# Performance work log

Measured on AMD Instinct MI355X. Metric: run time of the kernel, lower is better.

## Reference

```python
import jax, jax.numpy as jnp
import numpy as np

MAX_DIST = 5
D_PE = 16
NUM_ENTITIES = 50000
NUM_EDGES = 800000
NUM_ANCHOR_TRIPLES = 32
MAX_SOURCES = 2 * NUM_ANCHOR_TRIPLES  # upper bound on unique anchor entities


def setup_inputs() -> dict:
    key = jax.random.key(0)
    k1, k2, k3, k4 = jax.random.split(key, 4)
    h_ids = jax.random.randint(k1, (NUM_EDGES,), 0, NUM_ENTITIES)
    t_ids = jax.random.randint(k2, (NUM_EDGES,), 0, NUM_ENTITIES)
    anchor_triple_indices = jax.random.randint(k3, (NUM_ANCHOR_TRIPLES,), 0, NUM_EDGES)
    dist_embed = jax.random.normal(k4, (MAX_DIST + 1, D_PE), dtype=jnp.float32)
    return {
        "h_ids": h_ids,
        "t_ids": t_ids,
        "anchor_triple_indices": anchor_triple_indices,
        "num_entities": NUM_ENTITIES,
        "dist_embed": dist_embed,
    }


def _bfs_mean_counts(h_ids, t_ids, anchor_triple_indices, num_entities):
    """Returns [num_entities, MAX_DIST+1] mean one-hot distance counts over anchors."""
    # unique anchor entities, padded with -1 to a static size (torch.unique equivalent)
    anchor_ents = jnp.concatenate([h_ids[anchor_triple_indices], t_ids[anchor_triple_indices]])
    sources = jnp.unique(anchor_ents, size=MAX_SOURCES, fill_value=-1)  # [K], sorted
    valid = sources >= 0                                                # [K]
    src = jnp.where(valid, sources, 0)
    K = src.shape[0]
    col = jnp.arange(K)

    # symmetric adjacency as edge list (duplicates are harmless: only >0 is tested)
    edge_src = jnp.concatenate([h_ids, t_ids])  # [2E]
    edge_dst = jnp.concatenate([t_ids, h_ids])  # [2E]

    frontier = jnp.zeros((num_entities, K), jnp.float32).at[src, col].set(1.0)
    visited = jnp.zeros((num_entities, K), bool).at[src, col].set(True)
    dist = jnp.full((num_entities, K), MAX_DIST, jnp.int32).at[src, col].set(0)

    for depth in range(1, MAX_DIST + 1):  # fixed small hop count
        # sparse adj @ frontier == scatter-add of gathered frontier rows
        new_frontier = jax.ops.segment_sum(frontier[edge_src], edge_dst, num_segments=num_entities)
        newly = (new_frontier > 0) & ~visited
        dist = jnp.where(newly, depth, dist)
        visited = visited | newly
        frontier = newly.astype(jnp.float32)

    # masked mean over valid anchor sources, expressed as distance-count histogram
    w = valid.astype(jnp.float32)
    n_valid = jnp.maximum(w.sum(), 1.0)
    onehot = jax.nn.one_hot(dist, MAX_DIST + 1, dtype=jnp.float32)  # [N, K, D+1]
    counts = jnp.einsum('nkd,k->nd', onehot, w) / n_valid           # [N, D+1]
    return counts


def reference(h_ids, t_ids, anchor_triple_indices, num_entities, dist_embed):
    counts = _bfs_mean_counts(h_ids, t_ids, anchor_triple_indices, num_entities)
    # mean over sources of embed(dist) == counts @ embedding table
    return counts @ dist_embed  # [num_entities, d_pe]
```

## Files before the change

### kernel.cpp

```cpp
#include <hip/hip_runtime.h>
#include <hip/hip_bf16.h>

typedef unsigned long long u64;
typedef unsigned int u32;

#define MAXD 5
#define BSH  6
#define BN   64
#define PAD  16
#define NW   256
#define NTH  256
#define CAPG 2816
#define HEMPTY 0xFFFFFFFFu


__global__ void scatter_setup(const int* __restrict__ h, const int* __restrict__ t,
                              int E, u32* __restrict__ cursorpad,
                              u32* __restrict__ recs, int NB,
                              const int* __restrict__ anchor, int A,
                              u64* __restrict__ NFg, u32* __restrict__ srcPack,
                              int* __restrict__ nvalid) {
    extern __shared__ u32 sh[];
    u32* lh    = sh;
    u32* base  = sh + NB;
    u32* hsKey = sh + 2 * NB;
    u32* hsBit = hsKey + 128;
    int tid = threadIdx.x;

    for (int i = tid; i < NB; i += NTH) lh[i] = 0u;
    if (tid < 128) hsKey[tid] = HEMPTY;
    __syncthreads();

    if (tid < 64) {
        int K = 2 * A;
        int a_ = (tid < K) ? anchor[(tid < A) ? tid : (tid - A)] : 0;
        int my = (tid < K) ? ((tid < A) ? h[a_] : t[a_]) : -1;
        bool uniq = (tid < K);
        for (int j = 0; j < 64; ++j) {
            int o = __shfl(my, j, 64);
            if (j < tid && o == my) uniq = false;
        }
        u64 mask = __ballot(uniq);
        if (blockIdx.x == 0 && tid == 0) *nvalid = (int)__popcll(mask);
        if (uniq) {
            u32 slot = ((u32)my * 2654435761u) >> 25;
            while (atomicCAS(&hsKey[slot], HEMPTY, (u32)my) != HEMPTY)
                slot = (slot + 1) & 127u;
            hsBit[slot] = (u32)tid;
        }
        if (blockIdx.x == 0)
            srcPack[tid] = uniq ? (((u32)my << BSH) | (u32)tid) : HEMPTY;
    }
    __syncthreads();

    auto srcMask = [&](u32 src) -> u64 {
        u32 slot = (src * 2654435761u) >> 25;
        while (true) {
            u32 k = hsKey[slot];
            if (k == src) return 1ull << hsBit[slot];
            if (k == HEMPTY) return 0ull;
            slot = (slot + 1) & 127u;
        }
    };

    int stride = gridDim.x * NTH;
    int t0 = blockIdx.x * NTH + tid;
    for (int e = t0; e < E; e += stride) {
        u32 uu = (u32)h[e], vv = (u32)t[e];
        atomicAdd(&lh[vv >> BSH], 1u);
        atomicAdd(&lh[uu >> BSH], 1u);
    }
    __syncthreads();
    for (int i = tid; i < NB; i += NTH) {
        u32 c = lh[i];
        base[i] = c ? atomicAdd(&cursorpad[i * PAD], c) : 0u;
    }
    __syncthreads();
    for (int i = tid; i < NB; i += NTH) lh[i] = 0u;
    __syncthreads();
    for (int e = t0; e < E; e += stride) {
        u32 uu = (u32)h[e], vv = (u32)t[e];
        u32 b1 = vv >> BSH;
        u32 r1 = base[b1] + atomicAdd(&lh[b1], 1u);
        if (r1 < CAPG) recs[b1 * CAPG + r1] = (uu << BSH) | (vv & (BN - 1));
        u32 b2 = uu >> BSH;
        u32 r2 = base[b2] + atomicAdd(&lh[b2], 1u);
        if (r2 < CAPG) recs[b2 * CAPG + r2] = (vv << BSH) | (uu & (BN - 1));
        if (uu != vv) {
            u64 m1 = srcMask(uu);
            if (m1) atomicOr(&NFg[vv], m1);
            u64 m2 = srcMask(vv);
            if (m2) atomicOr(&NFg[uu], m2);
        }
    }
}

__global__ __launch_bounds__(NTH) void level12(
    const u32* __restrict__ recs, const u32* __restrict__ cursorpad,
    const u32* __restrict__ srcPack, const u64* __restrict__ NFg,
    u64* __restrict__ F2, u64* __restrict__ V, u64* __restrict__ CNT, int N) {
    __shared__ u64 NF[BN];
    __shared__ u32 srcL[64];
    int b = blockIdx.x, tid = threadIdx.x;
    u32 o0 = (u32)b * CAPG;
    u32 cnt = min(cursorpad[b * PAD], (u32)CAPG);
    if (tid < BN) NF[tid] = 0ull;
    if (tid < 64) srcL[tid] = srcPack[tid];
    __syncthreads();
    u32 r = tid;
    for (; r + 3u * NTH < cnt; r += 4u * NTH) {
        u32 c0 = recs[o0 + r],           c1 = recs[o0 + r + NTH];
        u32 c2 = recs[o0 + r + 2 * NTH], c3 = recs[o0 + r + 3 * NTH];
        u64 f0 = NFg[c0 >> BSH], f1 = NFg[c1 >> BSH];
        u64 f2 = NFg[c2 >> BSH], f3 = NFg[c3 >> BSH];
        if (f0) atomicOr(&NF[c0 & (BN - 1)], f0);
        if (f1) atomicOr(&NF[c1 & (BN - 1)], f1);
        if (f2) atomicOr(&NF[c2 & (BN - 1)], f2);
        if (f3) atomicOr(&NF[c3 & (BN - 1)], f3);
    }
    for (; r < cnt; r += NTH) {
        u32 c0 = recs[o0 + r];
        u64 f0 = NFg[c0 >> BSH];
        if (f0) atomicOr(&NF[c0 & (BN - 1)], f0);
    }
    __syncthreads();
    if (tid < BN) {
        int n = b * BN + tid;
        if (n < N) {
            u64 srcbit = 0ull;
            for (int k = 0; k < 64; ++k) {
                u32 p = srcL[k];
                if (p != HEMPTY && (int)(p >> BSH) == n)
                    srcbit |= 1ull << (p & (BN - 1));
            }
            u64 nf1 = NFg[n];
            u64 v1 = srcbit | nf1;
            u64 newly2 = NF[tid] & ~v1;
            V[n] = v1 | newly2;
            F2[n] = newly2;
            CNT[n] = (srcbit ? 1ull : 0ull)
                   | ((u64)__popcll(nf1) << 8)
                   | ((u64)__popcll(newly2) << 16);
        }
    }
}

__global__ __launch_bounds__(NTH) void level3(
    const u32* __restrict__ recs, const u32* __restrict__ cursorpad,
    const u64* __restrict__ Fin, u64* __restrict__ Fout,
    u64* __restrict__ V, u64* __restrict__ CNT, int N) {
    __shared__ u64 NF[BN];
    int b = blockIdx.x, tid = threadIdx.x;
    u32 o0 = (u32)b * CAPG;
    u32 cnt = min(cursorpad[b * PAD], (u32)CAPG);
    if (tid < BN) NF[tid] = 0ull;
    __syncthreads();
    u32 r = tid;
    for (; r + 3u * NTH < cnt; r += 4u * NTH) {
        u32 c0 = recs[o0 + r],           c1 = recs[o0 + r + NTH];
        u32 c2 = recs[o0 + r + 2 * NTH], c3 = recs[o0 + r + 3 * NTH];
        u64 f0 = Fin[c0 >> BSH], f1 = Fin[c1 >> BSH];
        u64 f2 = Fin[c2 >> BSH], f3 = Fin[c3 >> BSH];
        if (f0) atomicOr(&NF[c0 & (BN - 1)], f0);
        if (f1) atomicOr(&NF[c1 & (BN - 1)], f1);
        if (f2) atomicOr(&NF[c2 & (BN - 1)], f2);
        if (f3) atomicOr(&NF[c3 & (BN - 1)], f3);
    }
    for (; r < cnt; r += NTH) {
        u32 c0 = recs[o0 + r];
        u64 f0 = Fin[c0 >> BSH];
        if (f0) atomicOr(&NF[c0 & (BN - 1)], f0);
    }
    __syncthreads();
    if (tid < BN) {
        int n = b * BN + tid;
        if (n < N) {
            u64 vis = V[n];
            u64 newly = NF[tid] & ~vis;
            Fout[n] = newly;
            if (newly) {
                V[n] = vis | newly;
                CNT[n] += (u64)__popcll(newly) << 24;
            }
        }
    }
}

__global__ __launch_bounds__(NTH) void level4_fin(
    const u32* __restrict__ recs, const u32* __restrict__ cursorpad,
    const u64* __restrict__ Fin, const u64* __restrict__ V,
    const u64* __restrict__ CNT, const int* __restrict__ nvalid,
    const float* __restrict__ embed, float* __restrict__ out, int N) {
    __shared__ u64 NF[BN];
    int b = blockIdx.x, tid = threadIdx.x;
    u32 o0 = (u32)b * CAPG;
    u32 cnt = min(cursorpad[b * PAD], (u32)CAPG);
    if (tid < BN) NF[tid] = 0ull;
    __syncthreads();
    u32 r = tid;
    for (; r + 3u * NTH < cnt; r += 4u * NTH) {
        u32 c0 = recs[o0 + r],           c1 = recs[o0 + r + NTH];
        u32 c2 = recs[o0 + r + 2 * NTH], c3 = recs[o0 + r + 3 * NTH];
        u64 f0 = Fin[c0 >> BSH], f1 = Fin[c1 >> BSH];
        u64 f2 = Fin[c2 >> BSH], f3 = Fin[c3 >> BSH];
        if (f0) atomicOr(&NF[c0 & (BN - 1)], f0);
        if (f1) atomicOr(&NF[c1 & (BN - 1)], f1);
        if (f2) atomicOr(&NF[c2 & (BN - 1)], f2);
        if (f3) atomicOr(&NF[c3 & (BN - 1)], f3);
    }
    for (; r < cnt; r += NTH) {
        u32 c0 = recs[o0 + r];
        u64 f0 = Fin[c0 >> BSH];
        if (f0) atomicOr(&NF[c0 & (BN - 1)], f0);
    }
    __syncthreads();
    int nl = tid >> 2, q = tid & 3;
    int n = b * BN + nl;
    if (n >= N) return;
    u64 vis = V[n];
    int c4 = __popcll(NF[nl] & ~vis);
    u64 c = CNT[n];
    int nv = *nvalid;
    float inv = 1.0f / (float)(nv > 0 ? nv : 1);
    float cd[MAXD + 1];
    int total = c4;
#pragma unroll
    for (int d = 0; d < 4; ++d) {
        int x = (int)((c >> (8 * d)) & 0xffull);
        total += x;
        cd[d] = (float)x;
    }
    cd[4] = (float)c4;
    cd[5] = (float)(nv - total);

    const float4* e4 = (const float4*)embed;
    float4 acc = {0.f, 0.f, 0.f, 0.f};
#pragma unroll
    for (int d = 0; d <= MAXD; ++d) {
        float4 e = e4[d * 4 + q];
        acc.x += cd[d] * e.x; acc.y += cd[d] * e.y;
        acc.z += cd[d] * e.z; acc.w += cd[d] * e.w;
    }
    acc.x *= inv; acc.y *= inv; acc.z *= inv; acc.w *= inv;
    ((float4*)(out + (size_t)n * 16))[q] = acc;
}

extern "C" void kernel_launch(void* const* d_in, const int* in_sizes, int n_in,
                              void* d_out, int out_size, void* d_ws, size_t ws_size,
                              hipStream_t stream) {
    const int*   h      = (const int*)d_in[0];
    const int*   t      = (const int*)d_in[1];
    const int*   anchor = (const int*)d_in[2];
    const float* embed  = (const float*)d_in[4];
    float*       out    = (float*)d_out;

    int E = in_sizes[0];
    int A = in_sizes[2];
    int D = in_sizes[4] / (MAXD + 1);
    int N = out_size / D;
    int NB = (N + BN - 1) >> BSH;
    (void)D;

    u32* cursorpad = (u32*)d_ws;
    u64* NFg = (u64*)(cursorpad + (size_t)NB * PAD);
    u64* V   = NFg + N;
    u64* CNT = V + N;
    u64* F2  = CNT + N;
    u64* F3  = F2 + N;
    u32* srcPack = (u32*)(F3 + N);
    int* nvalid  = (int*)(srcPack + 64);
    u32* recs    = (u32*)(nvalid + 1);

    hipMemsetAsync(d_ws, 0, (size_t)NB * PAD * 4 + (size_t)N * 8, stream);

    scatter_setup<<<NW, NTH, (2 * NB + 256) * sizeof(u32), stream>>>(
        h, t, E, cursorpad, recs, NB, anchor, A, NFg, srcPack, nvalid);

    level12<<<NB, NTH, 0, stream>>>(recs, cursorpad, srcPack, NFg, F2, V, CNT, N);
    level3<<<NB, NTH, 0, stream>>>(recs, cursorpad, F2, F3, V, CNT, N);
    level4_fin<<<NB, NTH, 0, stream>>>(recs, cursorpad, F3, V, CNT, nvalid,
                                       embed, out, N);
}
```

Measured before the change: 151.4 us.

## Replace global-atomic bucket scatter with per-chunk shared-memory counting sort

The setup kernel now partitions edges into 512 chunks. Each chunk is counting-sorted by destination bucket in shared memory using a block-wide prefix scan, then written contiguously along with a per-chunk u16 segment offset table. This removes global atomic cursors, the padded cursor array and its memset, and the fixed per-bucket capacity. In exchange, each BFS level kernel must gather its bucket's records from all 512 chunks through short, scattered per-thread segment walks instead of coalesced unrolled streams.

Result: slower. 167.0 us (+10.3%).

```diff
diff --git a/kernel.cpp b/kernel.cpp
--- a/kernel.cpp
+++ b/kernel.cpp
@@ -3,31 +3,33 @@
 
 typedef unsigned long long u64;
 typedef unsigned int u32;
+typedef unsigned short u16;
 
 #define MAXD 5
 #define BSH  6
 #define BN   64
-#define PAD  16
-#define NW   256
+#define NW   512
 #define NTH  256
-#define CAPG 2816
+#define NBMAX 1024
 #define HEMPTY 0xFFFFFFFFu
 
 
-__global__ void scatter_setup(const int* __restrict__ h, const int* __restrict__ t,
-                              int E, u32* __restrict__ cursorpad,
-                              u32* __restrict__ recs, int NB,
-                              const int* __restrict__ anchor, int A,
-                              u64* __restrict__ NFg, u32* __restrict__ srcPack,
-                              int* __restrict__ nvalid) {
+__global__ __launch_bounds__(NTH) void chunk_sort(
+    const int* __restrict__ h, const int* __restrict__ t, int E, int CE, int CAPC,
+    int NB, u32* __restrict__ recs, u16* __restrict__ segtab,
+    const int* __restrict__ anchor, int A,
+    u64* __restrict__ NFg, u32* __restrict__ srcPack, int* __restrict__ nvalid) {
     extern __shared__ u32 sh[];
-    u32* lh    = sh;
-    u32* base  = sh + NB;
-    u32* hsKey = sh + 2 * NB;
+    u32* s     = sh;
+    u32* cur   = sh + NBMAX;
+    u32* hsKey = cur + NB;
     u32* hsBit = hsKey + 128;
-    int tid = threadIdx.x;
-
-    for (int i = tid; i < NB; i += NTH) lh[i] = 0u;
+    u32* buf   = hsBit + 128;
+    int tid = threadIdx.x, c = blockIdx.x;
+    int lo = c * CE, hi = min(E, lo + CE);
+    int nrec = 2 * (hi - lo);
+
+    for (int i = tid; i < NB; i += NTH) cur[i] = 0u;
     if (tid < 128) hsKey[tid] = HEMPTY;
     __syncthreads();
 
@@ -41,16 +43,49 @@
             if (j < tid && o == my) uniq = false;
         }
         u64 mask = __ballot(uniq);
-        if (blockIdx.x == 0 && tid == 0) *nvalid = (int)__popcll(mask);
+        if (c == 0 && tid == 0) *nvalid = (int)__popcll(mask);
         if (uniq) {
             u32 slot = ((u32)my * 2654435761u) >> 25;
             while (atomicCAS(&hsKey[slot], HEMPTY, (u32)my) != HEMPTY)
                 slot = (slot + 1) & 127u;
             hsBit[slot] = (u32)tid;
         }
-        if (blockIdx.x == 0)
+        if (c == 0)
             srcPack[tid] = uniq ? (((u32)my << BSH) | (u32)tid) : HEMPTY;
     }
+    __syncthreads();
+
+    for (int e = lo + tid; e < hi; e += NTH) {
+        u32 uu = (u32)h[e], vv = (u32)t[e];
+        atomicAdd(&cur[vv >> BSH], 1u);
+        atomicAdd(&cur[uu >> BSH], 1u);
+    }
+    __syncthreads();
+
+    for (int k = 0; k < NBMAX / NTH; ++k) {
+        int i = tid + NTH * k;
+        s[i] = (i < NB) ? cur[i] : 0u;
+    }
+    __syncthreads();
+    for (int d = 1; d < NBMAX; d <<= 1) {
+        u32 v0[NBMAX / NTH];
+#pragma unroll
+        for (int k = 0; k < NBMAX / NTH; ++k) {
+            int i = tid + NTH * k;
+            v0[k] = (i >= d) ? s[i - d] : 0u;
+        }
+        __syncthreads();
+#pragma unroll
+        for (int k = 0; k < NBMAX / NTH; ++k) s[tid + NTH * k] += v0[k];
+        __syncthreads();
+    }
+    for (int i = tid; i < NB; i += NTH) {
+        u32 excl = s[i] - cur[i];
+        s[i] = excl;
+        cur[i] = 0u;
+        segtab[c * (NB + 1) + i] = (u16)excl;
+    }
+    if (tid == 0) segtab[c * (NB + 1) + NB] = (u16)nrec;
     __syncthreads();
 
     auto srcMask = [&](u32 src) -> u64 {
@@ -63,29 +98,12 @@
         }
     };
 
-    int stride = gridDim.x * NTH;
-    int t0 = blockIdx.x * NTH + tid;
-    for (int e = t0; e < E; e += stride) {
-        u32 uu = (u32)h[e], vv = (u32)t[e];
-        atomicAdd(&lh[vv >> BSH], 1u);
-        atomicAdd(&lh[uu >> BSH], 1u);
-    }
-    __syncthreads();
-    for (int i = tid; i < NB; i += NTH) {
-        u32 c = lh[i];
-        base[i] = c ? atomicAdd(&cursorpad[i * PAD], c) : 0u;
-    }
-    __syncthreads();
-    for (int i = tid; i < NB; i += NTH) lh[i] = 0u;
-    __syncthreads();
-    for (int e = t0; e < E; e += stride) {
+    for (int e = lo + tid; e < hi; e += NTH) {
         u32 uu = (u32)h[e], vv = (u32)t[e];
         u32 b1 = vv >> BSH;
-        u32 r1 = base[b1] + atomicAdd(&lh[b1], 1u);
-        if (r1 < CAPG) recs[b1 * CAPG + r1] = (uu << BSH) | (vv & (BN - 1));
+        buf[s[b1] + atomicAdd(&cur[b1], 1u)] = (uu << BSH) | (vv & (BN - 1));
         u32 b2 = uu >> BSH;
-        u32 r2 = base[b2] + atomicAdd(&lh[b2], 1u);
-        if (r2 < CAPG) recs[b2 * CAPG + r2] = (vv << BSH) | (uu & (BN - 1));
+        buf[s[b2] + atomicAdd(&cur[b2], 1u)] = (vv << BSH) | (uu & (BN - 1));
         if (uu != vv) {
             u64 m1 = srcMask(uu);
             if (m1) atomicOr(&NFg[vv], m1);
@@ -93,35 +111,31 @@
             if (m2) atomicOr(&NFg[uu], m2);
         }
     }
-}
+    __syncthreads();
+
+    for (int i = tid; i < nrec; i += NTH) recs[c * CAPC + i] = buf[i];
+}
+
 
 __global__ __launch_bounds__(NTH) void level12(
-    const u32* __restrict__ recs, const u32* __restrict__ cursorpad,
+    const u32* __restrict__ recs, const u16* __restrict__ segtab, int CAPC, int NB,
     const u32* __restrict__ srcPack, const u64* __restrict__ NFg,
     u64* __restrict__ F2, u64* __restrict__ V, u64* __restrict__ CNT, int N) {
     __shared__ u64 NF[BN];
     __shared__ u32 srcL[64];
     int b = blockIdx.x, tid = threadIdx.x;
-    u32 o0 = (u32)b * CAPG;
-    u32 cnt = min(cursorpad[b * PAD], (u32)CAPG);
     if (tid < BN) NF[tid] = 0ull;
     if (tid < 64) srcL[tid] = srcPack[tid];
     __syncthreads();
-    u32 r = tid;
-    for (; r + 3u * NTH < cnt; r += 4u * NTH) {
-        u32 c0 = recs[o0 + r],           c1 = recs[o0 + r + NTH];
-        u32 c2 = recs[o0 + r + 2 * NTH], c3 = recs[o0 + r + 3 * NTH];
-        u64 f0 = NFg[c0 >> BSH], f1 = NFg[c1 >> BSH];
-        u64 f2 = NFg[c2 >> BSH], f3 = NFg[c3 >> BSH];
-        if (f0) atomicOr(&NF[c0 & (BN - 1)], f0);
-        if (f1) atomicOr(&NF[c1 & (BN - 1)], f1);
-        if (f2) atomicOr(&NF[c2 & (BN - 1)], f2);
-        if (f3) atomicOr(&NF[c3 & (BN - 1)], f3);
-    }
-    for (; r < cnt; r += NTH) {
-        u32 c0 = recs[o0 + r];
-        u64 f0 = NFg[c0 >> BSH];
-        if (f0) atomicOr(&NF[c0 & (BN - 1)], f0);
+    for (int c = tid; c < NW; c += NTH) {
+        const u16* st = segtab + c * (NB + 1);
+        u32 base = (u32)c * CAPC;
+        u32 k = st[b], k1 = st[b + 1];
+        for (; k < k1; ++k) {
+            u32 rec = recs[base + k];
+            u64 f = NFg[rec >> BSH];
+            if (f) atomicOr(&NF[rec & (BN - 1)], f);
+        }
     }
     __syncthreads();
     if (tid < BN) {
@@ -146,30 +160,22 @@
 }
 
 __global__ __launch_bounds__(NTH) void level3(
-    const u32* __restrict__ recs, const u32* __restrict__ cursorpad,
+    const u32* __restrict__ recs, const u16* __restrict__ segtab, int CAPC, int NB,
     const u64* __restrict__ Fin, u64* __restrict__ Fout,
     u64* __restrict__ V, u64* __restrict__ CNT, int N) {
     __shared__ u64 NF[BN];
     int b = blockIdx.x, tid = threadIdx.x;
-    u32 o0 = (u32)b * CAPG;
-    u32 cnt = min(cursorpad[b * PAD], (u32)CAPG);
     if (tid < BN) NF[tid] = 0ull;
     __syncthreads();
-    u32 r = tid;
-    for (; r + 3u * NTH < cnt; r += 4u * NTH) {
-        u32 c0 = recs[o0 + r],           c1 = recs[o0 + r + NTH];
-        u32 c2 = recs[o0 + r + 2 * NTH], c3 = recs[o0 + r + 3 * NTH];
-        u64 f0 = Fin[c0 >> BSH], f1 = Fin[c1 >> BSH];
-        u64 f2 = Fin[c2 >> BSH], f3 = Fin[c3 >> BSH];
-        if (f0) atomicOr(&NF[c0 & (BN - 1)], f0);
-        if (f1) atomicOr(&NF[c1 & (BN - 1)], f1);
-        if (f2) atomicOr(&NF[c2 & (BN - 1)], f2);
-        if (f3) atomicOr(&NF[c3 & (BN - 1)], f3);
-    }
-    for (; r < cnt; r += NTH) {
-        u32 c0 = recs[o0 + r];
-        u64 f0 = Fin[c0 >> BSH];
-        if (f0) atomicOr(&NF[c0 & (BN - 1)], f0);
+    for (int c = tid; c < NW; c += NTH) {
+        const u16* st = segtab + c * (NB + 1);
+        u32 base = (u32)c * CAPC;
+        u32 k = st[b], k1 = st[b + 1];
+        for (; k < k1; ++k) {
+            u32 rec = recs[base + k];
+            u64 f = Fin[rec >> BSH];
+            if (f) atomicOr(&NF[rec & (BN - 1)], f);
+        }
     }
     __syncthreads();
     if (tid < BN) {
@@ -187,31 +193,23 @@
 }
 
 __global__ __launch_bounds__(NTH) void level4_fin(
-    const u32* __restrict__ recs, const u32* __restrict__ cursorpad,
+    const u32* __restrict__ recs, const u16* __restrict__ segtab, int CAPC, int NB,
     const u64* __restrict__ Fin, const u64* __restrict__ V,
     const u64* __restrict__ CNT, const int* __restrict__ nvalid,
     const float* __restrict__ embed, float* __restrict__ out, int N) {
     __shared__ u64 NF[BN];
     int b = blockIdx.x, tid = threadIdx.x;
-    u32 o0 = (u32)b * CAPG;
-    u32 cnt = min(cursorpad[b * PAD], (u32)CAPG);
     if (tid < BN) NF[tid] = 0ull;
     __syncthreads();
-    u32 r = tid;
-    for (; r + 3u * NTH < cnt; r += 4u * NTH) {
-        u32 c0 = recs[o0 + r],           c1 = recs[o0 + r + NTH];
-        u32 c2 = recs[o0 + r + 2 * NTH], c3 = recs[o0 + r + 3 * NTH];
-        u64 f0 = Fin[c0 >> BSH], f1 = Fin[c1 >> BSH];
-        u64 f2 = Fin[c2 >> BSH], f3 = Fin[c3 >> BSH];
-        if (f0) atomicOr(&NF[c0 & (BN - 1)], f0);
-        if (f1) atomicOr(&NF[c1 & (BN - 1)], f1);
-        if (f2) atomicOr(&NF[c2 & (BN - 1)], f2);
-        if (f3) atomicOr(&NF[c3 & (BN - 1)], f3);
-    }
-    for (; r < cnt; r += NTH) {
-        u32 c0 = recs[o0 + r];
-        u64 f0 = Fin[c0 >> BSH];
-        if (f0) atomicOr(&NF[c0 & (BN - 1)], f0);
+    for (int c = tid; c < NW; c += NTH) {
+        const u16* st = segtab + c * (NB + 1);
+        u32 base = (u32)c * CAPC;
+        u32 k = st[b], k1 = st[b + 1];
+        for (; k < k1; ++k) {
+            u32 rec = recs[base + k];
+            u64 f = Fin[rec >> BSH];
+            if (f) atomicOr(&NF[rec & (BN - 1)], f);
+        }
     }
     __syncthreads();
     int nl = tid >> 2, q = tid & 3;
@@ -259,10 +257,11 @@
     int D = in_sizes[4] / (MAXD + 1);
     int N = out_size / D;
     int NB = (N + BN - 1) >> BSH;
+    int CE = (E + NW - 1) / NW;
+    int CAPC = 2 * CE;
     (void)D;
 
-    u32* cursorpad = (u32*)d_ws;
-    u64* NFg = (u64*)(cursorpad + (size_t)NB * PAD);
+    u64* NFg = (u64*)d_ws;
     u64* V   = NFg + N;
     u64* CNT = V + N;
     u64* F2  = CNT + N;
@@ -270,14 +269,17 @@
     u32* srcPack = (u32*)(F3 + N);
     int* nvalid  = (int*)(srcPack + 64);
     u32* recs    = (u32*)(nvalid + 1);
-
-    hipMemsetAsync(d_ws, 0, (size_t)NB * PAD * 4 + (size_t)N * 8, stream);
-
-    scatter_setup<<<NW, NTH, (2 * NB + 256) * sizeof(u32), stream>>>(
-        h, t, E, cursorpad, recs, NB, anchor, A, NFg, srcPack, nvalid);
-
-    level12<<<NB, NTH, 0, stream>>>(recs, cursorpad, srcPack, NFg, F2, V, CNT, N);
-    level3<<<NB, NTH, 0, stream>>>(recs, cursorpad, F2, F3, V, CNT, N);
-    level4_fin<<<NB, NTH, 0, stream>>>(recs, cursorpad, F3, V, CNT, nvalid,
-                                       embed, out, N);
-}
+    u16* segtab  = (u16*)(recs + (size_t)NW * CAPC);
+
+    hipMemsetAsync(NFg, 0, (size_t)N * 8, stream);
+
+    size_t shmem = (NBMAX + NB + 256) * sizeof(u32) + (size_t)CAPC * sizeof(u32);
+    chunk_sort<<<NW, NTH, shmem, stream>>>(h, t, E, CE, CAPC, NB, recs, segtab,
+                                           anchor, A, NFg, srcPack, nvalid);
+
+    level12<<<NB, NTH, 0, stream>>>(recs, segtab, CAPC, NB, srcPack, NFg,
+                                    F2, V, CNT, N);
+    level3<<<NB, NTH, 0, stream>>>(recs, segtab, CAPC, NB, F2, F3, V, CNT, N);
+    level4_fin<<<NB, NTH, 0, stream>>>(recs, segtab, CAPC, NB, F3, V, CNT,
+                                       nvalid, embed, out, N);
+}
```
